# Performance work log

Hardware: AMD Instinct MI355X
Metric: run time of the kernel (lower is better)

Reference implementation:

```python
import jax, jax.numpy as jnp
import numpy as np

GRID_SIZE = 5
SPLINE_ORDER = 3
NUM_EXPERTS = 8
TOP_K = 2
CAP_FACTOR = 1.25
TEMP = 1.0
GDHW = (4, 4, 4)


def make_grid(in_features):
    # efficient-KAN grid buffer: grid_range=[-1,1], extended by spline_order on each side
    h = 2.0 / GRID_SIZE
    g = jnp.arange(-SPLINE_ORDER, GRID_SIZE + SPLINE_ORDER + 1, dtype=jnp.float32) * h - 1.0
    return jnp.broadcast_to(g, (in_features, g.shape[0]))


def b_splines(x, grid):
    # x: (N, in) -> (N, in, GRID_SIZE + SPLINE_ORDER) Cox-de Boor bases
    x = x[:, :, None]
    bases = ((x >= grid[:, :-1]) & (x < grid[:, 1:])).astype(x.dtype)
    for k in range(1, SPLINE_ORDER + 1):
        left = (x - grid[:, : -(k + 1)]) / (grid[:, k:-1] - grid[:, : -(k + 1)])
        right = (grid[:, k + 1:] - x) / (grid[:, k + 1:] - grid[:, 1:-k])
        bases = left * bases[:, :, :-1] + right * bases[:, :, 1:]
    return bases


def kan_linear(x, base_w, spline_w, scaler, grid):
    base = jax.nn.silu(x) @ base_w.T
    bs = b_splines(x, grid)                                   # (N, in, coef)
    spline = jnp.einsum('nic,oic->no', bs, spline_w * scaler[:, :, None])
    return base + spline


def layernorm(x, w, b, eps=1e-5):
    mu = x.mean(-1, keepdims=True)
    var = x.var(-1, keepdims=True)
    return (x - mu) / jnp.sqrt(var + eps) * w + b


def setup_inputs() -> dict:
    key = jax.random.key(0)
    ks = jax.random.split(key, 12)
    Cf, hidden, E, nc = 256, 170, NUM_EXPERTS, 2
    coef = GRID_SIZE + SPLINE_ORDER
    def nrm(k, shape, scale):
        return jax.random.normal(k, shape, dtype=jnp.float32) * scale
    return {
        'fpn_feat': nrm(ks[0], (8, 254, 32, 32, 32), 1.0),
        'seg_logits': nrm(ks[1], (8, 2, 32, 32, 32), 1.0),
        'ln_r_w': jnp.ones((Cf,), jnp.float32),
        'ln_r_b': jnp.zeros((Cf,), jnp.float32),
        'ln_h_w': jnp.ones((Cf,), jnp.float32),
        'ln_h_b': jnp.zeros((Cf,), jnp.float32),
        'router_w': nrm(ks[2], (E, Cf), Cf ** -0.5),
        'router_b': jnp.zeros((E,), jnp.float32),
        'bw1': nrm(ks[3], (E, hidden, Cf), Cf ** -0.5),
        'sw1': nrm(ks[4], (E, hidden, Cf, coef), 0.1 * Cf ** -0.5),
        'sc1': nrm(ks[5], (E, hidden, Cf), Cf ** -0.5),
        'bw2': nrm(ks[6], (E, Cf, hidden), hidden ** -0.5),
        'sw2': nrm(ks[7], (E, Cf, hidden, coef), 0.1 * hidden ** -0.5),
        'sc2': nrm(ks[8], (E, Cf, hidden), hidden ** -0.5),
        'cls_bw': nrm(ks[9], (nc, Cf), Cf ** -0.5),
        'cls_sw': nrm(ks[10], (nc, Cf, coef), 0.1 * Cf ** -0.5),
        'cls_sc': nrm(ks[11], (nc, Cf), Cf ** -0.5),
        'grid_cf': make_grid(Cf),
        'grid_hid': make_grid(hidden),
    }


def reference(fpn_feat, seg_logits, ln_r_w, ln_r_b, ln_h_w, ln_h_b,
              router_w, router_b, bw1, sw1, sc1, bw2, sw2, sc2,
              cls_bw, cls_sw, cls_sc, grid_cf, grid_hid):
    fused = jnp.concatenate([fpn_feat, seg_logits], axis=1)   # (B, Cf, D, H, W)
    B, C, D, H, W = fused.shape
    gd, gh, gw = GDHW
    dp, hp, wp = D // gd, H // gh, W // gw
    # split into gd*gh*gw blocks per sample
    blk = fused.reshape(B, C, gd, dp, gh, hp, gw, wp)
    blk = blk.transpose(0, 2, 4, 6, 1, 3, 5, 7).reshape(-1, C, dp, hp, wp)
    vec = blk.mean(axis=(2, 3, 4))                            # (N, Cf) global avg pool

    N = vec.shape[0]
    E = NUM_EXPERTS
    x_norm = layernorm(vec, ln_r_w, ln_r_b)
    scores = (x_norm @ router_w.T + router_b) / TEMP          # (N, E)
    top_val, top_idx = jax.lax.top_k(scores, TOP_K)
    top_w = jax.nn.softmax(top_val, axis=-1)
    capacity = int(CAP_FACTOR * N * TOP_K / E) + 1

    onehot = top_idx[None] == jnp.arange(E)[:, None, None]    # (E, N, K)
    sel = onehot.any(-1)                                      # (E, N)
    pos = jnp.cumsum(sel.astype(jnp.int32), axis=1)           # rank among selected (1-based)
    keep = sel & (pos <= capacity)                            # capacity drop = first-come order
    w = (top_w[None] * onehot.astype(top_w.dtype)).sum(-1)    # (E, N) combine weights

    def expert(bw1e, sw1e, sc1e, bw2e, sw2e, sc2e):
        h = kan_linear(x_norm, bw1e, sw1e, sc1e, grid_cf)
        h = jax.nn.gelu(h, approximate=False)                 # torch nn.GELU default (erf)
        return kan_linear(h, bw2e, sw2e, sc2e, grid_hid)

    y_all = jax.vmap(expert)(bw1, sw1, sc1, bw2, sw2, sc2)    # (E, N, Cf)
    out = jnp.einsum('en,enc->nc', keep.astype(vec.dtype) * w, y_all)

    conf = scores.max(-1)                                     # (N,)
    logits_blk = kan_linear(layernorm(out, ln_h_w, ln_h_b), cls_bw, cls_sw, cls_sc, grid_cf)
    P = gd * gh * gw
    weight = jax.nn.softmax(conf.reshape(B, P), axis=-1)[:, :, None]
    logits = (logits_blk.reshape(B, P, -1) * weight).sum(1)   # (B, num_classes)
    return logits
```

## Files before the change

### kernel.cpp

```cpp
#include <hip/hip_runtime.h>
#include <math.h>

#define CF 256
#define HID 170
#define NE 8
#define NTOK 512
#define K1 2304
#define K2P 1536
#define CAPACITY 161

typedef __bf16 bf16x8 __attribute__((ext_vector_type(8)));
typedef unsigned short u16x8 __attribute__((ext_vector_type(8)));
typedef float f32x4 __attribute__((ext_vector_type(4)));

__device__ __forceinline__ float silu_f(float x) { return x / (1.0f + expf(-x)); }
__device__ __forceinline__ float gelu_f(float x) {
    return 0.5f * x * (1.0f + erff(x * 0.70710678118654752f));
}

__device__ __forceinline__ unsigned short f2bf(float f) {
    unsigned int u = __float_as_uint(f);
    u = u + 0x7fffu + ((u >> 16) & 1u);
    return (unsigned short)(u >> 16);
}

__device__ __forceinline__ void gl_lds16(const unsigned short* g, unsigned short* l) {
    __builtin_amdgcn_global_load_lds(
        (const __attribute__((address_space(1))) unsigned int*)g,
        (__attribute__((address_space(3))) unsigned int*)l, 16, 0, 0);
}

__device__ __forceinline__ void bspline8(float x, float bs[8]) {
    float b[11];
#pragma unroll
    for (int j = 0; j < 11; ++j) {
        float g0 = (float)(j - 3) * 0.4f - 1.0f;
        float g1 = (float)(j - 2) * 0.4f - 1.0f;
        b[j] = (x >= g0 && x < g1) ? 1.0f : 0.0f;
    }
#pragma unroll
    for (int k = 1; k <= 3; ++k) {
        float inv = 2.5f / (float)k;
#pragma unroll
        for (int j = 0; j < 10 - (k - 1); ++j) {
            float gj   = (float)(j - 3) * 0.4f - 1.0f;
            float gjk1 = (float)(j - 2 + k) * 0.4f - 1.0f;
            b[j] = (x - gj) * inv * b[j] + (gjk1 - x) * inv * b[j + 1];
        }
    }
#pragma unroll
    for (int c = 0; c < 8; ++c) bs[c] = b[c];
}

__global__ __launch_bounds__(256) void mega_front_kernel(const float* __restrict__ fpn,
                                                         const float* __restrict__ seg,
                                                         const float* __restrict__ bw1,
                                                         const float* __restrict__ sw1,
                                                         const float* __restrict__ sc1,
                                                         const float* __restrict__ bw2,
                                                         const float* __restrict__ sw2,
                                                         const float* __restrict__ sc2,
                                                         float* __restrict__ vec,
                                                         unsigned short* __restrict__ W1,
                                                         unsigned short* __restrict__ W2,
                                                         float* __restrict__ out) {
    int id = blockIdx.x, tid = threadIdx.x;
    if (id == 2048 && tid < 16) out[tid] = 0.0f;
    if (id < 2048) {
        int c = id & 255, b = id >> 8;
        const float* src = (c < 254) ? fpn + (size_t)(b * 254 + c) * 32768
                                     : seg + (size_t)(b * 2 + (c - 254)) * 32768;
        const float4* s4 = (const float4*)src;
        float s[4] = {0.f, 0.f, 0.f, 0.f};
#pragma unroll
        for (int it = 0; it < 32; ++it) {
            float4 v = s4[it * 256 + tid];
            s[it >> 3] += v.x + v.y + v.z + v.w;
        }
        __shared__ float acc[64];
        if (tid < 64) acc[tid] = 0.0f;
        __syncthreads();
        int bh = tid >> 6, bw = (tid & 7) >> 1;
#pragma unroll
        for (int bd = 0; bd < 4; ++bd) atomicAdd(&acc[bd * 16 + bh * 4 + bw], s[bd]);
        __syncthreads();
        if (tid < 64) vec[(size_t)(b * 64 + tid) * CF + c] = acc[tid] * (1.0f / 512.0f);
    } else if (id < 2048 + NE * HID) {
        int r = id - 2048;
        int o = r % HID, e = r / HID, i = tid;
        size_t oi = (size_t)(e * HID + o) * CF + i;
        unsigned short* row = W1 + (size_t)(e * HID + o) * K1;
        row[i] = f2bf(bw1[oi]);
        float sc = sc1[oi];
        const float* sw = sw1 + oi * 8;
        u16x8 pk;
#pragma unroll
        for (int c = 0; c < 8; ++c) pk[c] = f2bf(sw[c] * sc);
        *(u16x8*)(row + CF + i * 8) = pk;
    } else {
        int r = id - (2048 + NE * HID);
        int o = r & 255, e = r >> 8, t = tid;
        unsigned short* row = W2 + (size_t)(e * CF + o) * K2P;
        if (t < HID) {
            size_t oi = (size_t)(e * CF + o) * HID + t;
            row[t] = f2bf(bw2[oi]);
            float sc = sc2[oi];
            const float* sw = sw2 + oi * 8;
            u16x8 pk;
#pragma unroll
            for (int c = 0; c < 8; ++c) pk[c] = f2bf(sw[c] * sc);
            *(u16x8*)(row + HID + t * 8) = pk;
        } else if (t < HID + 6) {
            row[HID * 9 + (t - HID)] = 0;
        }
    }
}

__global__ __launch_bounds__(256) void ln_score_a1_kernel(const float* __restrict__ vec,
                                                          const float* __restrict__ lnw,
                                                          const float* __restrict__ lnb,
                                                          const float* __restrict__ rw,
                                                          const float* __restrict__ rb,
                                                          float* __restrict__ scores,
                                                          unsigned short* __restrict__ A1,
                                                          unsigned short* __restrict__ A2) {
    int n = blockIdx.x, i = threadIdx.x;
    if (i < 48) {
        int e = i / 6, j = i - e * 6;
        A2[((size_t)e * NTOK + n) * K2P + HID * 9 + j] = 0;
    }
    float v = vec[(size_t)n * CF + i];
    float s1 = v, s2 = v * v;
#pragma unroll
    for (int off = 32; off > 0; off >>= 1) {
        s1 += __shfl_xor(s1, off);
        s2 += __shfl_xor(s2, off);
    }
    __shared__ float rs1[4], rs2[4];
    int lane = i & 63, wid = i >> 6;
    if (lane == 0) { rs1[wid] = s1; rs2[wid] = s2; }
    __syncthreads();
    float tot1 = rs1[0] + rs1[1] + rs1[2] + rs1[3];
    float tot2 = rs2[0] + rs2[1] + rs2[2] + rs2[3];
    float mu = tot1 * (1.0f / CF);
    float var = tot2 * (1.0f / CF) - mu * mu;
    float rsd = rsqrtf(var + 1e-5f);
    float xv = (v - mu) * rsd * lnw[i] + lnb[i];
    unsigned short* r = A1 + (size_t)n * K1;
    r[i] = f2bf(silu_f(xv));
    float bs[8]; bspline8(xv, bs);
    u16x8 pk;
#pragma unroll
    for (int c = 0; c < 8; ++c) pk[c] = f2bf(bs[c]);
    *(u16x8*)(r + CF + i * 8) = pk;
    float p[NE];
#pragma unroll
    for (int e = 0; e < NE; ++e) p[e] = xv * rw[e * CF + i];
#pragma unroll
    for (int off = 32; off > 0; off >>= 1)
#pragma unroll
        for (int e = 0; e < NE; ++e) p[e] += __shfl_xor(p[e], off);
    __shared__ float pacc[4][NE];
    if (lane == 0)
#pragma unroll
        for (int e = 0; e < NE; ++e) pacc[wid][e] = p[e];
    __syncthreads();
    if (i < NE)
        scores[n * NE + i] = pacc[0][i] + pacc[1][i] + pacc[2][i] + pacc[3][i] + rb[i];
}

__global__ __launch_bounds__(256) void gemm_mfma_kernel(
        const unsigned short* __restrict__ Ag, const unsigned short* __restrict__ Bg,
        float* __restrict__ C, unsigned short* __restrict__ A2,
        const float* __restrict__ scores, float* __restrict__ cw, float* __restrict__ conf,
        int N, int K, long sA, long sB, long sC, int ldc, int mode) {
    __shared__ alignas(16) unsigned short As[2][4096];
    __shared__ alignas(16) unsigned short Bs[2][4096];
    __shared__ int   ti0[NTOK], ti1[NTOK];
    __shared__ float tw0[NTOK], tw1[NTOK];

    int tid = threadIdx.x;
    if (mode == 1 && blockIdx.x == 3) {
        if (blockIdx.y != 0 || blockIdx.z != 0) return;
        int lane = tid & 63, w4 = tid >> 6;
#pragma unroll
        for (int half = 0; half < 2; ++half) {
            int n = half * 256 + tid;
            float m1 = -1e30f, m2 = -1e30f; int i1 = 0, i2 = 0;
#pragma unroll
            for (int e = 0; e < NE; ++e) {
                float sc = scores[n * NE + e];
                if (sc > m1) { m2 = m1; i2 = i1; m1 = sc; i1 = e; }
                else if (sc > m2) { m2 = sc; i2 = e; }
            }
            conf[n] = m1;
            float ew = expf(m2 - m1);
            ti0[n] = i1; ti1[n] = i2;
            tw0[n] = 1.0f / (1.0f + ew); tw1[n] = ew / (1.0f + ew);
        }
        __syncthreads();
#pragma unroll
        for (int e2 = 0; e2 < 2; ++e2) {
            int e = w4 * 2 + e2;
            int cnt = 0;
#pragma unroll
            for (int c = 0; c < NTOK / 64; ++c) {
                int t = c * 64 + lane;
                int h0 = (ti0[t] == e), h1 = (ti1[t] == e);
                int sel = h0 | h1;
                unsigned long long mask = __ballot(sel);
                int pos = cnt + (int)__popcll(mask & ((1ull << lane) - 1ull));
                float wv = 0.f;
                if (sel && pos < CAPACITY) wv = h0 ? tw0[t] : tw1[t];
                cw[e * NTOK + t] = wv;
                cnt += (int)__popcll(mask);
            }
        }
        return;
    }

    int e = blockIdx.z;
    const unsigned short* A = Ag + (size_t)e * sA;
    const unsigned short* B = Bg + (size_t)e * sB;
    int m0 = blockIdx.y * 64, n0 = blockIdx.x * 64;
    int lane = tid & 63, w = tid >> 6;
    int wr = w >> 1, wc = w & 1;
    int fr = lane & 15, fg = lane >> 4;
    int lrow = lane >> 3, lch = lane & 7;
    int csw = (lch ^ lrow) * 8;

    const unsigned short* aS0 = A + (size_t)(m0 + w * 16 + lrow) * K + csw;
    const unsigned short* aS1 = aS0 + (size_t)8 * K;
    const unsigned short* bS0 = B + (size_t)(n0 + w * 16 + lrow) * K + csw;
    const unsigned short* bS1 = bS0 + (size_t)8 * K;
    unsigned short* dA0[2] = {&As[0][(w * 16) * 64], &As[1][(w * 16) * 64]};
    unsigned short* dA1[2] = {&As[0][(w * 16 + 8) * 64], &As[1][(w * 16 + 8) * 64]};
    unsigned short* dB0[2] = {&Bs[0][(w * 16) * 64], &Bs[1][(w * 16) * 64]};
    unsigned short* dB1[2] = {&Bs[0][(w * 16 + 8) * 64], &Bs[1][(w * 16 + 8) * 64]};

#define STAGE(bi, k0)                 \
    gl_lds16(aS0 + (k0), dA0[bi]);    \
    gl_lds16(aS1 + (k0), dA1[bi]);    \
    gl_lds16(bS0 + (k0), dB0[bi]);    \
    gl_lds16(bS1 + (k0), dB1[bi]);

    f32x4 acc[2][2];
#pragma unroll
    for (int i = 0; i < 2; ++i)
#pragma unroll
        for (int j = 0; j < 2; ++j)
#pragma unroll
            for (int r = 0; r < 4; ++r) acc[i][j][r] = 0.f;

    const int steps = K >> 6;
    STAGE(0, 0);
    for (int s = 0; s < steps; ++s) {
        int bi = s & 1;
        if (s + 1 < steps) {
            STAGE(bi ^ 1, (s + 1) << 6);
            asm volatile("s_waitcnt vmcnt(4)" ::: "memory");
        } else {
            asm volatile("s_waitcnt vmcnt(0)" ::: "memory");
        }
        __builtin_amdgcn_s_barrier();
        asm volatile("" ::: "memory");
        const unsigned char* Ab = (const unsigned char*)As[bi];
        const unsigned char* Bb = (const unsigned char*)Bs[bi];
#pragma unroll
        for (int ks = 0; ks < 2; ++ks) {
            int kb = ks * 64 + fg * 16;
            u16x8 af[2], bf[2];
#pragma unroll
            for (int mf = 0; mf < 2; ++mf) {
                int row = wr * 32 + mf * 16 + fr;
                af[mf] = *(const u16x8*)(Ab + row * 128 + (kb ^ ((row & 7) << 4)));
            }
#pragma unroll
            for (int nf = 0; nf < 2; ++nf) {
                int row = wc * 32 + nf * 16 + fr;
                bf[nf] = *(const u16x8*)(Bb + row * 128 + (kb ^ ((row & 7) << 4)));
            }
#pragma unroll
            for (int mf = 0; mf < 2; ++mf)
#pragma unroll
                for (int nf = 0; nf < 2; ++nf)
                    acc[mf][nf] = __builtin_amdgcn_mfma_f32_16x16x32_bf16(
                        __builtin_bit_cast(bf16x8, af[mf]),
                        __builtin_bit_cast(bf16x8, bf[nf]), acc[mf][nf], 0, 0, 0);
        }
        asm volatile("" ::: "memory");
        __builtin_amdgcn_s_barrier();
        asm volatile("" ::: "memory");
    }
#undef STAGE

    if (mode == 1) {
#pragma unroll
        for (int mf = 0; mf < 2; ++mf)
#pragma unroll
            for (int nf = 0; nf < 2; ++nf)
#pragma unroll
                for (int r = 0; r < 4; ++r) {
                    int row = m0 + wr * 32 + mf * 16 + fg * 4 + r;
                    int col = n0 + wc * 32 + nf * 16 + fr;
                    if (col < N) {
                        float g = gelu_f(acc[mf][nf][r]);
                        unsigned short* rr = A2 + ((size_t)e * NTOK + row) * K2P;
                        rr[col] = f2bf(silu_f(g));
                        float bs[8]; bspline8(g, bs);
                        u16x8 pk;
#pragma unroll
                        for (int c = 0; c < 8; ++c) pk[c] = f2bf(bs[c]);
                        *(u16x8*)(rr + HID + col * 8) = pk;
                    }
                }
    } else {
        float* Ce = C + (size_t)e * sC;
#pragma unroll
        for (int mf = 0; mf < 2; ++mf)
#pragma unroll
            for (int nf = 0; nf < 2; ++nf)
#pragma unroll
                for (int r = 0; r < 4; ++r) {
                    int row = m0 + wr * 32 + mf * 16 + fg * 4 + r;
                    int col = n0 + wc * 32 + nf * 16 + fr;
                    if (col < N) Ce[(size_t)row * ldc + col] = acc[mf][nf][r];
                }
    }
}

__global__ __launch_bounds__(256) void combcls_kernel(const float* __restrict__ y,
                                                      const float* __restrict__ cw,
                                                      const float* __restrict__ conf,
                                                      const float* __restrict__ lnw,
                                                      const float* __restrict__ lnb,
                                                      const float* __restrict__ cbw,
                                                      const float* __restrict__ csw,
                                                      const float* __restrict__ csc,
                                                      float* __restrict__ out) {
    int n = blockIdx.x, i = threadIdx.x;
    float v = 0.f;
#pragma unroll
    for (int e = 0; e < NE; ++e)
        v += cw[e * NTOK + n] * y[((size_t)(e * NTOK + n)) * CF + i];
    float s1 = v, s2 = v * v;
#pragma unroll
    for (int off = 32; off > 0; off >>= 1) {
        s1 += __shfl_xor(s1, off);
        s2 += __shfl_xor(s2, off);
    }
    __shared__ float rA[4], rB[4], rP0[4], rP1[4];
    int lane = i & 63, wid = i >> 6;
    if (lane == 0) { rA[wid] = s1; rB[wid] = s2; }
    __syncthreads();
    float tot1 = rA[0] + rA[1] + rA[2] + rA[3];
    float tot2 = rB[0] + rB[1] + rB[2] + rB[3];
    float mu = tot1 * (1.0f / CF);
    float var = tot2 * (1.0f / CF) - mu * mu;
    float rs = rsqrtf(var + 1e-5f);
    float xh = (v - mu) * rs * lnw[i] + lnb[i];
    float si = silu_f(xh);
    float bs[8]; bspline8(xh, bs);
    float p0 = si * cbw[i], p1 = si * cbw[CF + i];
    float sp0 = 0.f, sp1 = 0.f;
#pragma unroll
    for (int c = 0; c < 8; ++c) {
        sp0 += bs[c] * csw[(size_t)i * 8 + c];
        sp1 += bs[c] * csw[(size_t)(CF + i) * 8 + c];
    }
    p0 += sp0 * csc[i];
    p1 += sp1 * csc[CF + i];
#pragma unroll
    for (int off = 32; off > 0; off >>= 1) {
        p0 += __shfl_xor(p0, off);
        p1 += __shfl_xor(p1, off);
    }
    if (lane == 0) { rP0[wid] = p0; rP1[wid] = p1; }
// ... 15 lines not shown
            atomicAdd(&out[b * 2 + 0], wself * l0);
            atomicAdd(&out[b * 2 + 1], wself * l1);
        }
    }
}

extern "C" void kernel_launch(void* const* d_in, const int* in_sizes, int n_in,
                              void* d_out, int out_size, void* d_ws, size_t ws_size,
                              hipStream_t stream) {
    const float* fpn      = (const float*)d_in[0];
    const float* seg      = (const float*)d_in[1];
    const float* ln_r_w   = (const float*)d_in[2];
    const float* ln_r_b   = (const float*)d_in[3];
    const float* ln_h_w   = (const float*)d_in[4];
    const float* ln_h_b   = (const float*)d_in[5];
    const float* router_w = (const float*)d_in[6];
    const float* router_b = (const float*)d_in[7];
    const float* bw1      = (const float*)d_in[8];
    const float* sw1      = (const float*)d_in[9];
    const float* sc1      = (const float*)d_in[10];
    const float* bw2      = (const float*)d_in[11];
    const float* sw2      = (const float*)d_in[12];
    const float* sc2      = (const float*)d_in[13];
    const float* cls_bw   = (const float*)d_in[14];
    const float* cls_sw   = (const float*)d_in[15];
    const float* cls_sc   = (const float*)d_in[16];
    float* out = (float*)d_out;

    float* ws = (float*)d_ws;
    float* vec    = ws;
    float* scores = vec + 131072;
    float* cw     = scores + 4096;
    float* conf   = cw + 4096;
    float* yall   = conf + 512;
    unsigned short* A1b = (unsigned short*)(yall + 1048576);
    unsigned short* W1b = A1b + (size_t)NTOK * K1;
    unsigned short* A2b = W1b + (size_t)NE * HID * K1;
    unsigned short* W2b = A2b + (size_t)NE * NTOK * K2P;

    mega_front_kernel<<<dim3(2048 + NE * HID + 2048), dim3(256), 0, stream>>>(
        fpn, seg, bw1, sw1, sc1, bw2, sw2, sc2, vec, W1b, W2b, out);
    ln_score_a1_kernel<<<dim3(NTOK), dim3(256), 0, stream>>>(vec, ln_r_w, ln_r_b, router_w,
                                                             router_b, scores, A1b, A2b);
    gemm_mfma_kernel<<<dim3(4, 8, NE), dim3(256), 0, stream>>>(
        A1b, W1b, nullptr, A2b, scores, cw, conf, HID, K1, 0L, (long)HID * K1, 0L, 0, 1);
    gemm_mfma_kernel<<<dim3(4, 8, NE), dim3(256), 0, stream>>>(
        A2b, W2b, yall, nullptr, nullptr, nullptr, nullptr, CF, K2P, (long)NTOK * K2P,
        (long)CF * K2P, (long)NTOK * CF, CF, 0);
    combcls_kernel<<<dim3(NTOK), dim3(256), 0, stream>>>(yall, cw, conf, ln_h_w, ln_h_b,
                                                         cls_bw, cls_sw, cls_sc, out);
}
```

Before: 133.3 us.

## Split-K expert GEMMs in halves and move routing into last LN block

Both expert GEMMs now split K into two halves across the z grid dimension, which doubles the block count. Each half writes fp32 partials. In the first GEMM, the second-arriving block (found with an atomic counter) sums both halves and applies GELU plus B-spline expansion. The second GEMM's halves are summed inside the combine kernel. The top-2 routing and capacity computation moves out of a GEMM block into the last-finishing block of the LN/score kernel. The GEMM staging switches from direct global-to-LDS loads to register prefetch with single-buffered LDS. The aim is better CU occupancy on the small GEMMs, at the cost of extra partial-sum traffic, atomics and threadfences.

```diff
diff --git a/kernel.cpp b/kernel.cpp
--- a/kernel.cpp
+++ b/kernel.cpp
@@ -8,6 +8,8 @@
 #define K1 2304
 #define K2P 1536
 #define CAPACITY 161
+#define KH1 1152
+#define KH2 768
 
 typedef __bf16 bf16x8 __attribute__((ext_vector_type(8)));
 typedef unsigned short u16x8 __attribute__((ext_vector_type(8)));
@@ -22,12 +24,6 @@
     unsigned int u = __float_as_uint(f);
     u = u + 0x7fffu + ((u >> 16) & 1u);
     return (unsigned short)(u >> 16);
-}
-
-__device__ __forceinline__ void gl_lds16(const unsigned short* g, unsigned short* l) {
-    __builtin_amdgcn_global_load_lds(
-        (const __attribute__((address_space(1))) unsigned int*)g,
-        (__attribute__((address_space(3))) unsigned int*)l, 16, 0, 0);
 }
 
 __device__ __forceinline__ void bspline8(float x, float bs[8]) {
@@ -63,9 +59,13 @@
                                                          float* __restrict__ vec,
                                                          unsigned short* __restrict__ W1,
                                                          unsigned short* __restrict__ W2,
+                                                         int* __restrict__ cnts,
                                                          float* __restrict__ out) {
     int id = blockIdx.x, tid = threadIdx.x;
-    if (id == 2048 && tid < 16) out[tid] = 0.0f;
+    if (id == 2048) {
+        if (tid < 16) out[tid] = 0.0f;
+        cnts[tid] = 0;
+    }
     if (id < 2048) {
         int c = id & 255, b = id >> 8;
         const float* src = (c < 254) ? fpn + (size_t)(b * 254 + c) * 32768
@@ -123,7 +123,10 @@
                                                           const float* __restrict__ rb,
                                                           float* __restrict__ scores,
                                                           unsigned short* __restrict__ A1,
-                                                          unsigned short* __restrict__ A2) {
+                                                          unsigned short* __restrict__ A2,
+                                                          int* __restrict__ lncnt,
+                                                          float* __restrict__ cw,
+                                                          float* __restrict__ conf) {
     int n = blockIdx.x, i = threadIdx.x;
     if (i < 48) {
         int e = i / 6, j = i - e * 6;
@@ -167,82 +170,75 @@
     __syncthreads();
     if (i < NE)
         scores[n * NE + i] = pacc[0][i] + pacc[1][i] + pacc[2][i] + pacc[3][i] + rb[i];
+    __syncthreads();
+    __shared__ int lastf;
+    if (i == 0) {
+        __threadfence();
+        lastf = (atomicAdd(lncnt, 1) == NTOK - 1);
+        __threadfence();
+    }
+    __syncthreads();
+    if (!lastf) return;
+    __shared__ int   ti0[NTOK], ti1[NTOK];
+    __shared__ float tw0[NTOK], tw1[NTOK];
+#pragma unroll
+    for (int half = 0; half < 2; ++half) {
+        int t = half * 256 + i;
+        float m1 = -1e30f, m2 = -1e30f; int i1 = 0, i2 = 0;
+#pragma unroll
+        for (int e = 0; e < NE; ++e) {
+            float sc = scores[t * NE + e];
+            if (sc > m1) { m2 = m1; i2 = i1; m1 = sc; i1 = e; }
+            else if (sc > m2) { m2 = sc; i2 = e; }
+        }
+        conf[t] = m1;
+        float ew = expf(m2 - m1);
+        ti0[t] = i1; ti1[t] = i2;
+        tw0[t] = 1.0f / (1.0f + ew); tw1[t] = ew / (1.0f + ew);
+    }
+    __syncthreads();
+    int w4 = i >> 6;
+#pragma unroll
+    for (int e2 = 0; e2 < 2; ++e2) {
+        int e = w4 * 2 + e2;
+        int cnt = 0;
+#pragma unroll
+        for (int c = 0; c < NTOK / 64; ++c) {
+            int t = c * 64 + lane;
+            int h0 = (ti0[t] == e), h1 = (ti1[t] == e);
+            int sel = h0 | h1;
+            unsigned long long mask = __ballot(sel);
+            int pos = cnt + (int)__popcll(mask & ((1ull << lane) - 1ull));
+            float wv = 0.f;
+            if (sel && pos < CAPACITY) wv = h0 ? tw0[t] : tw1[t];
+            cw[e * NTOK + t] = wv;
+            cnt += (int)__popcll(mask);
+        }
+    }
 }
 
 __global__ __launch_bounds__(256) void gemm_mfma_kernel(
         const unsigned short* __restrict__ Ag, const unsigned short* __restrict__ Bg,
-        float* __restrict__ C, unsigned short* __restrict__ A2,
-        const float* __restrict__ scores, float* __restrict__ cw, float* __restrict__ conf,
-        int N, int K, long sA, long sB, long sC, int ldc, int mode) {
-    __shared__ alignas(16) unsigned short As[2][4096];
-    __shared__ alignas(16) unsigned short Bs[2][4096];
-    __shared__ int   ti0[NTOK], ti1[NTOK];
-    __shared__ float tw0[NTOK], tw1[NTOK];
+        float* __restrict__ Ppart, unsigned short* __restrict__ A2,
+        int* __restrict__ cnt, int N, int LD, long sA, long sB, long pStride,
+        int khalf, int mode) {
+    int z = blockIdx.z, e = z >> 1, half = z & 1;
+    int koff = half * khalf, steps = khalf >> 6;
+    const unsigned short* A = Ag + (size_t)e * sA + koff;
+    const unsigned short* B = Bg + (size_t)e * sB + koff;
+    int m0 = blockIdx.y * 64, n0 = blockIdx.x * 64;
+
+    __shared__ alignas(16) unsigned char AsB[8192];
+    __shared__ alignas(16) unsigned char BsB[8192];
 
     int tid = threadIdx.x;
-    if (mode == 1 && blockIdx.x == 3) {
-        if (blockIdx.y != 0 || blockIdx.z != 0) return;
-        int lane = tid & 63, w4 = tid >> 6;
-#pragma unroll
-        for (int half = 0; half < 2; ++half) {
-            int n = half * 256 + tid;
-            float m1 = -1e30f, m2 = -1e30f; int i1 = 0, i2 = 0;
-#pragma unroll
-            for (int e = 0; e < NE; ++e) {
-                float sc = scores[n * NE + e];
-                if (sc > m1) { m2 = m1; i2 = i1; m1 = sc; i1 = e; }
-                else if (sc > m2) { m2 = sc; i2 = e; }
-            }
-            conf[n] = m1;
-            float ew = expf(m2 - m1);
-            ti0[n] = i1; ti1[n] = i2;
-            tw0[n] = 1.0f / (1.0f + ew); tw1[n] = ew / (1.0f + ew);
-        }
-        __syncthreads();
-#pragma unroll
-        for (int e2 = 0; e2 < 2; ++e2) {
-            int e = w4 * 2 + e2;
-            int cnt = 0;
-#pragma unroll
-            for (int c = 0; c < NTOK / 64; ++c) {
-                int t = c * 64 + lane;
-                int h0 = (ti0[t] == e), h1 = (ti1[t] == e);
-                int sel = h0 | h1;
-                unsigned long long mask = __ballot(sel);
-                int pos = cnt + (int)__popcll(mask & ((1ull << lane) - 1ull));
-                float wv = 0.f;
-                if (sel && pos < CAPACITY) wv = h0 ? tw0[t] : tw1[t];
-                cw[e * NTOK + t] = wv;
-                cnt += (int)__popcll(mask);
-            }
-        }
-        return;
-    }
-
-    int e = blockIdx.z;
-    const unsigned short* A = Ag + (size_t)e * sA;
-    const unsigned short* B = Bg + (size_t)e * sB;
-    int m0 = blockIdx.y * 64, n0 = blockIdx.x * 64;
     int lane = tid & 63, w = tid >> 6;
     int wr = w >> 1, wc = w & 1;
     int fr = lane & 15, fg = lane >> 4;
-    int lrow = lane >> 3, lch = lane & 7;
-    int csw = (lch ^ lrow) * 8;
-
-    const unsigned short* aS0 = A + (size_t)(m0 + w * 16 + lrow) * K + csw;
-    const unsigned short* aS1 = aS0 + (size_t)8 * K;
-    const unsigned short* bS0 = B + (size_t)(n0 + w * 16 + lrow) * K + csw;
-    const unsigned short* bS1 = bS0 + (size_t)8 * K;
-    unsigned short* dA0[2] = {&As[0][(w * 16) * 64], &As[1][(w * 16) * 64]};
-    unsigned short* dA1[2] = {&As[0][(w * 16 + 8) * 64], &As[1][(w * 16 + 8) * 64]};
-    unsigned short* dB0[2] = {&Bs[0][(w * 16) * 64], &Bs[1][(w * 16) * 64]};
-    unsigned short* dB1[2] = {&Bs[0][(w * 16 + 8) * 64], &Bs[1][(w * 16 + 8) * 64]};
-
-#define STAGE(bi, k0)                 \
-    gl_lds16(aS0 + (k0), dA0[bi]);    \
-    gl_lds16(aS1 + (k0), dA1[bi]);    \
-    gl_lds16(bS0 + (k0), dB0[bi]);    \
-    gl_lds16(bS1 + (k0), dB1[bi]);
+    int srow = tid >> 3, schunk = tid & 7;
+    int r0 = srow, r1 = srow + 32;
+    int wb0 = r0 * 128 + ((schunk * 16) ^ ((r0 & 7) << 4));
+    int wb1 = r1 * 128 + ((schunk * 16) ^ ((r1 & 7) << 4));
 
     f32x4 acc[2][2];
 #pragma unroll
@@ -252,20 +248,32 @@
 #pragma unroll
             for (int r = 0; r < 4; ++r) acc[i][j][r] = 0.f;
 
-    const int steps = K >> 6;
-    STAGE(0, 0);
+    int bn0 = n0 + r0, bn1 = n0 + r1;
+    const unsigned short* Ar0 = A + (size_t)(m0 + r0) * LD + schunk * 8;
+    const unsigned short* Ar1 = A + (size_t)(m0 + r1) * LD + schunk * 8;
+    const unsigned short* Br0 = B + (size_t)bn0 * LD + schunk * 8;
+    const unsigned short* Br1 = B + (size_t)bn1 * LD + schunk * 8;
+    u16x8 a0, a1, b0, b1;
+    a0 = *(const u16x8*)Ar0;
+    a1 = *(const u16x8*)Ar1;
+    b0 = b1 = (u16x8){0, 0, 0, 0, 0, 0, 0, 0};
+    if (bn0 < N) b0 = *(const u16x8*)Br0;
+    if (bn1 < N) b1 = *(const u16x8*)Br1;
+
     for (int s = 0; s < steps; ++s) {
-        int bi = s & 1;
+        __syncthreads();
+        *(u16x8*)(AsB + wb0) = a0;
+        *(u16x8*)(AsB + wb1) = a1;
+        *(u16x8*)(BsB + wb0) = b0;
+        *(u16x8*)(BsB + wb1) = b1;
+        __syncthreads();
         if (s + 1 < steps) {
-            STAGE(bi ^ 1, (s + 1) << 6);
-            asm volatile("s_waitcnt vmcnt(4)" ::: "memory");
-        } else {
-            asm volatile("s_waitcnt vmcnt(0)" ::: "memory");
-        }
-        __builtin_amdgcn_s_barrier();
-        asm volatile("" ::: "memory");
-        const unsigned char* Ab = (const unsigned char*)As[bi];
-        const unsigned char* Bb = (const unsigned char*)Bs[bi];
+            int k0 = (s + 1) << 6;
+            a0 = *(const u16x8*)(Ar0 + k0);
+            a1 = *(const u16x8*)(Ar1 + k0);
+            if (bn0 < N) b0 = *(const u16x8*)(Br0 + k0);
+            if (bn1 < N) b1 = *(const u16x8*)(Br1 + k0);
+        }
 #pragma unroll
         for (int ks = 0; ks < 2; ++ks) {
             int kb = ks * 64 + fg * 16;
@@ -273,12 +281,12 @@
 #pragma unroll
             for (int mf = 0; mf < 2; ++mf) {
                 int row = wr * 32 + mf * 16 + fr;
-                af[mf] = *(const u16x8*)(Ab + row * 128 + (kb ^ ((row & 7) << 4)));
+                af[mf] = *(const u16x8*)(AsB + row * 128 + (kb ^ ((row & 7) << 4)));
             }
 #pragma unroll
             for (int nf = 0; nf < 2; ++nf) {
                 int row = wc * 32 + nf * 16 + fr;
-                bf[nf] = *(const u16x8*)(Bb + row * 128 + (kb ^ ((row & 7) << 4)));
+                bf[nf] = *(const u16x8*)(BsB + row * 128 + (kb ^ ((row & 7) << 4)));
             }
 #pragma unroll
             for (int mf = 0; mf < 2; ++mf)
@@ -288,48 +296,55 @@
                         __builtin_bit_cast(bf16x8, af[mf]),
                         __builtin_bit_cast(bf16x8, bf[nf]), acc[mf][nf], 0, 0, 0);
         }
-        asm volatile("" ::: "memory");
-        __builtin_amdgcn_s_barrier();
-        asm volatile("" ::: "memory");
-    }
-#undef STAGE
-
-    if (mode == 1) {
-#pragma unroll
-        for (int mf = 0; mf < 2; ++mf)
-#pragma unroll
-            for (int nf = 0; nf < 2; ++nf)
-#pragma unroll
-                for (int r = 0; r < 4; ++r) {
-                    int row = m0 + wr * 32 + mf * 16 + fg * 4 + r;
-                    int col = n0 + wc * 32 + nf * 16 + fr;
-                    if (col < N) {
-                        float g = gelu_f(acc[mf][nf][r]);
-                        unsigned short* rr = A2 + ((size_t)e * NTOK + row) * K2P;
-                        rr[col] = f2bf(silu_f(g));
-                        float bs[8]; bspline8(g, bs);
-                        u16x8 pk;
-#pragma unroll
-                        for (int c = 0; c < 8; ++c) pk[c] = f2bf(bs[c]);
-                        *(u16x8*)(rr + HID + col * 8) = pk;
-                    }
+    }
+
+    float* P = Ppart + (size_t)half * pStride + (size_t)e * NTOK * N;
+#pragma unroll
+    for (int mf = 0; mf < 2; ++mf)
+#pragma unroll
+        for (int nf = 0; nf < 2; ++nf)
+#pragma unroll
+            for (int r = 0; r < 4; ++r) {
+                int row = m0 + wr * 32 + mf * 16 + fg * 4 + r;
+                int col = n0 + wc * 32 + nf * 16 + fr;
+                if (col < N) P[(size_t)row * N + col] = acc[mf][nf][r];
+            }
+    if (mode == 0) return;
+
+    __syncthreads();
+    __shared__ int lastf;
+    int tix = e * 24 + blockIdx.y * 3 + blockIdx.x;
+    if (tid == 0) {
+        __threadfence();
+        lastf = (atomicAdd(&cnt[tix], 1) == 1);
+        __threadfence();
+    }
+    __syncthreads();
+    if (!lastf) return;
+    const float* Q = Ppart + (size_t)(half ^ 1) * pStride + (size_t)e * NTOK * N;
+#pragma unroll
+    for (int mf = 0; mf < 2; ++mf)
+#pragma unroll
+        for (int nf = 0; nf < 2; ++nf)
+#pragma unroll
+            for (int r = 0; r < 4; ++r) {
+                int row = m0 + wr * 32 + mf * 16 + fg * 4 + r;
+                int col = n0 + wc * 32 + nf * 16 + fr;
+                if (col < N) {
+                    float g = gelu_f(acc[mf][nf][r] + Q[(size_t)row * N + col]);
+                    unsigned short* rr = A2 + ((size_t)e * NTOK + row) * K2P;
+                    rr[col] = f2bf(silu_f(g));
+                    float bs[8]; bspline8(g, bs);
+                    u16x8 pk;
+#pragma unroll
+                    for (int c = 0; c < 8; ++c) pk[c] = f2bf(bs[c]);
+                    *(u16x8*)(rr + HID + col * 8) = pk;
                 }
-    } else {
-        float* Ce = C + (size_t)e * sC;
-#pragma unroll
-        for (int mf = 0; mf < 2; ++mf)
-#pragma unroll
-            for (int nf = 0; nf < 2; ++nf)
-#pragma unroll
-                for (int r = 0; r < 4; ++r) {
-                    int row = m0 + wr * 32 + mf * 16 + fg * 4 + r;
-                    int col = n0 + wc * 32 + nf * 16 + fr;
-                    if (col < N) Ce[(size_t)row * ldc + col] = acc[mf][nf][r];
-                }
-    }
-}
-
-__global__ __launch_bounds__(256) void combcls_kernel(const float* __restrict__ y,
+            }
+}
+
+__global__ __launch_bounds__(256) void combcls_kernel(const float* __restrict__ y0,
+                                                      const float* __restrict__ y1,
                                                       const float* __restrict__ cw,
                                                       const float* __restrict__ conf,
                                                       const float* __restrict__ lnw,
@@ -341,8 +356,10 @@
     int n = blockIdx.x, i = threadIdx.x;
     float v = 0.f;
 #pragma unroll
-    for (int e = 0; e < NE; ++e)
-        v += cw[e * NTOK + n] * y[((size_t)(e * NTOK + n)) * CF + i];
+    for (int e = 0; e < NE; ++e) {
+        size_t idx = ((size_t)(e * NTOK + n)) * CF + i;
+        v += cw[e * NTOK + n] * (y0[idx] + y1[idx]);
+    }
     float s1 = v, s2 = v * v;
 #pragma unroll
     for (int off = 32; off > 0; off >>= 1) {
@@ -424,21 +441,25 @@
     float* scores = vec + 131072;
     float* cw     = scores + 4096;
     float* conf   = cw + 4096;
-    float* yall   = conf + 512;
-    unsigned short* A1b = (unsigned short*)(yall + 1048576);
+    int*   cnts   = (int*)(conf + 512);
+    float* Hpart  = (float*)(cnts + 256);
+    float* Ypart  = Hpart + 2 * (size_t)NE * NTOK * HID;
+    unsigned short* A1b = (unsigned short*)(Ypart + 2 * (size_t)NE * NTOK * CF);
     unsigned short* W1b = A1b + (size_t)NTOK * K1;
     unsigned short* A2b = W1b + (size_t)NE * HID * K1;
     unsigned short* W2b = A2b + (size_t)NE * NTOK * K2P;
 
     mega_front_kernel<<<dim3(2048 + NE * HID + 2048), dim3(256), 0, stream>>>(
-        fpn, seg, bw1, sw1, sc1, bw2, sw2, sc2, vec, W1b, W2b, out);
-    ln_score_a1_kernel<<<dim3(NTOK), dim3(256), 0, stream>>>(vec, ln_r_w, ln_r_b, router_w,
-                                                             router_b, scores, A1b, A2b);
-    gemm_mfma_kernel<<<dim3(4, 8, NE), dim3(256), 0, stream>>>(
-        A1b, W1b, nullptr, A2b, scores, cw, conf, HID, K1, 0L, (long)HID * K1, 0L, 0, 1);
-    gemm_mfma_kernel<<<dim3(4, 8, NE), dim3(256), 0, stream>>>(
-        A2b, W2b, yall, nullptr, nullptr, nullptr, nullptr, CF, K2P, (long)NTOK * K2P,
-        (long)CF * K2P, (long)NTOK * CF, CF, 0);
-    combcls_kernel<<<dim3(NTOK), dim3(256), 0, stream>>>(yall, cw, conf, ln_h_w, ln_h_b,
-                                                         cls_bw, cls_sw, cls_sc, out);
-}
+        fpn, seg, bw1, sw1, sc1, bw2, sw2, sc2, vec, W1b, W2b, cnts, out);
+    ln_score_a1_kernel<<<dim3(NTOK), dim3(256), 0, stream>>>(
+        vec, ln_r_w, ln_r_b, router_w, router_b, scores, A1b, A2b, cnts + 192, cw, conf);
+    gemm_mfma_kernel<<<dim3(3, 8, 16), dim3(256), 0, stream>>>(
+        A1b, W1b, Hpart, A2b, cnts, HID, K1, 0L, (long)HID * K1,
+        (long)NE * NTOK * HID, KH1, 1);
+    gemm_mfma_kernel<<<dim3(4, 8, 16), dim3(256), 0, stream>>>(
+        A2b, W2b, Ypart, nullptr, nullptr, CF, K2P, (long)NTOK * K2P, (long)CF * K2P,
+        (long)NE * NTOK * CF, KH2, 0);
+    combcls_kernel<<<dim3(NTOK), dim3(256), 0, stream>>>(
+        Ypart, Ypart + (size_t)NE * NTOK * CF, cw, conf, ln_h_w, ln_h_b, cls_bw, cls_sw,
+        cls_sc, out);
+}
```

Measured after the change: 168.3 us. +26.2%, slower.

## Retile expert GEMMs to 32x64 blocks with register-staged loads

Applied to the files above, without the earlier changes.

Reshapes both expert GEMMs from 64x64 tiles with 256 threads to 32x64 tiles with 128 threads on a flat 1D grid. This gives more blocks to fill the GPU's compute units and removes the wasted fourth column tile in the first GEMM, where N is 170. The direct global-to-LDS async loads with a double buffer are replaced by register prefetch into a single LDS buffer, with two barriers per k-step. The kernel is templated on mode, and routing now runs in one extra block. The trade-offs are more barriers, no LDS double buffering, and more total A-tile reloads.

```diff
diff --git a/kernel.cpp b/kernel.cpp
--- a/kernel.cpp
+++ b/kernel.cpp
@@ -22,12 +22,6 @@
     unsigned int u = __float_as_uint(f);
     u = u + 0x7fffu + ((u >> 16) & 1u);
     return (unsigned short)(u >> 16);
-}
-
-__device__ __forceinline__ void gl_lds16(const unsigned short* g, unsigned short* l) {
-    __builtin_amdgcn_global_load_lds(
-        (const __attribute__((address_space(1))) unsigned int*)g,
-        (__attribute__((address_space(3))) unsigned int*)l, 16, 0, 0);
 }
 
 __device__ __forceinline__ void bspline8(float x, float bs[8]) {
@@ -169,39 +163,40 @@
         scores[n * NE + i] = pacc[0][i] + pacc[1][i] + pacc[2][i] + pacc[3][i] + rb[i];
 }
 
-__global__ __launch_bounds__(256) void gemm_mfma_kernel(
+template <int MODE>
+__global__ __launch_bounds__(128) void gemm_mfma_kernel(
         const unsigned short* __restrict__ Ag, const unsigned short* __restrict__ Bg,
         float* __restrict__ C, unsigned short* __restrict__ A2,
         const float* __restrict__ scores, float* __restrict__ cw, float* __restrict__ conf,
-        int N, int K, long sA, long sB, long sC, int ldc, int mode) {
-    __shared__ alignas(16) unsigned short As[2][4096];
-    __shared__ alignas(16) unsigned short Bs[2][4096];
-    __shared__ int   ti0[NTOK], ti1[NTOK];
-    __shared__ float tw0[NTOK], tw1[NTOK];
-
-    int tid = threadIdx.x;
-    if (mode == 1 && blockIdx.x == 3) {
-        if (blockIdx.y != 0 || blockIdx.z != 0) return;
-        int lane = tid & 63, w4 = tid >> 6;
-#pragma unroll
-        for (int half = 0; half < 2; ++half) {
-            int n = half * 256 + tid;
+        int N, int K, long sA, long sB, long sC, int ldc, int ntx, int grid_main) {
+    __shared__ alignas(16) unsigned char smem[12288];
+    int bid = blockIdx.x, tid = threadIdx.x;
+    int lane = tid & 63, w = tid >> 6;
+
+    if (MODE == 1 && bid >= grid_main) {
+        int* ti0 = (int*)smem;
+        int* ti1 = ti0 + NTOK;
+        float* tw0 = (float*)(ti1 + NTOK);
+        float* tw1 = tw0 + NTOK;
+#pragma unroll
+        for (int q = 0; q < 4; ++q) {
+            int t = q * 128 + tid;
             float m1 = -1e30f, m2 = -1e30f; int i1 = 0, i2 = 0;
 #pragma unroll
             for (int e = 0; e < NE; ++e) {
-                float sc = scores[n * NE + e];
+                float sc = scores[t * NE + e];
                 if (sc > m1) { m2 = m1; i2 = i1; m1 = sc; i1 = e; }
                 else if (sc > m2) { m2 = sc; i2 = e; }
             }
-            conf[n] = m1;
+            conf[t] = m1;
             float ew = expf(m2 - m1);
-            ti0[n] = i1; ti1[n] = i2;
-            tw0[n] = 1.0f / (1.0f + ew); tw1[n] = ew / (1.0f + ew);
+            ti0[t] = i1; ti1[t] = i2;
+            tw0[t] = 1.0f / (1.0f + ew); tw1[t] = ew / (1.0f + ew);
         }
         __syncthreads();
 #pragma unroll
-        for (int e2 = 0; e2 < 2; ++e2) {
-            int e = w4 * 2 + e2;
+        for (int eh = 0; eh < 4; ++eh) {
+            int e = w * 4 + eh;
             int cnt = 0;
 #pragma unroll
             for (int c = 0; c < NTOK / 64; ++c) {
@@ -219,30 +214,33 @@
         return;
     }
 
-    int e = blockIdx.z;
-    const unsigned short* A = Ag + (size_t)e * sA;
-    const unsigned short* B = Bg + (size_t)e * sB;
-    int m0 = blockIdx.y * 64, n0 = blockIdx.x * 64;
-    int lane = tid & 63, w = tid >> 6;
-    int wr = w >> 1, wc = w & 1;
+    int tpe = 16 * ntx;
+    int e = bid / tpe, rem = bid % tpe;
+    int m0 = (rem / ntx) * 32, n0 = (rem % ntx) * 64;
+    const unsigned short* A = Ag + (size_t)e * sA + (size_t)m0 * K;
+    const unsigned short* B = Bg + (size_t)e * sB + (size_t)n0 * K;
+
+    unsigned char* AsB = smem;
+    unsigned char* BsB = smem + 4096;
+
     int fr = lane & 15, fg = lane >> 4;
-    int lrow = lane >> 3, lch = lane & 7;
-    int csw = (lch ^ lrow) * 8;
-
-    const unsigned short* aS0 = A + (size_t)(m0 + w * 16 + lrow) * K + csw;
-    const unsigned short* aS1 = aS0 + (size_t)8 * K;
-    const unsigned short* bS0 = B + (size_t)(n0 + w * 16 + lrow) * K + csw;
-    const unsigned short* bS1 = bS0 + (size_t)8 * K;
-    unsigned short* dA0[2] = {&As[0][(w * 16) * 64], &As[1][(w * 16) * 64]};
-    unsigned short* dA1[2] = {&As[0][(w * 16 + 8) * 64], &As[1][(w * 16 + 8) * 64]};
-    unsigned short* dB0[2] = {&Bs[0][(w * 16) * 64], &Bs[1][(w * 16) * 64]};
-    unsigned short* dB1[2] = {&Bs[0][(w * 16 + 8) * 64], &Bs[1][(w * 16 + 8) * 64]};
-
-#define STAGE(bi, k0)                 \
-    gl_lds16(aS0 + (k0), dA0[bi]);    \
-    gl_lds16(aS1 + (k0), dA1[bi]);    \
-    gl_lds16(bS0 + (k0), dB0[bi]);    \
-    gl_lds16(bS1 + (k0), dB1[bi]);
+    int aw[2], bw[4];
+    const unsigned short* aSrc[2];
+    const unsigned short* bSrc[4];
+    bool bOk[4];
+#pragma unroll
+    for (int q = 0; q < 2; ++q) {
+        int c = tid + q * 128, r = c >> 3, ch = c & 7;
+        aw[q] = r * 128 + ((ch * 16) ^ ((r & 7) << 4));
+        aSrc[q] = A + (size_t)r * K + ch * 8;
+    }
+#pragma unroll
+    for (int q = 0; q < 4; ++q) {
+        int c = tid + q * 128, r = c >> 3, ch = c & 7;
+        bw[q] = r * 128 + ((ch * 16) ^ ((r & 7) << 4));
+        bSrc[q] = B + (size_t)r * K + ch * 8;
+        bOk[q] = (n0 + r) < N;
+    }
 
     f32x4 acc[2][2];
 #pragma unroll
@@ -253,32 +251,41 @@
             for (int r = 0; r < 4; ++r) acc[i][j][r] = 0.f;
 
     const int steps = K >> 6;
-    STAGE(0, 0);
+    u16x8 pa[2], pb[4];
+#pragma unroll
+    for (int q = 0; q < 2; ++q) pa[q] = *(const u16x8*)aSrc[q];
+#pragma unroll
+    for (int q = 0; q < 4; ++q)
+        pb[q] = bOk[q] ? *(const u16x8*)bSrc[q] : (u16x8){0, 0, 0, 0, 0, 0, 0, 0};
+
     for (int s = 0; s < steps; ++s) {
-        int bi = s & 1;
+        __syncthreads();
+#pragma unroll
+        for (int q = 0; q < 2; ++q) *(u16x8*)(AsB + aw[q]) = pa[q];
+#pragma unroll
+        for (int q = 0; q < 4; ++q) *(u16x8*)(BsB + bw[q]) = pb[q];
+        __syncthreads();
         if (s + 1 < steps) {
-            STAGE(bi ^ 1, (s + 1) << 6);
-            asm volatile("s_waitcnt vmcnt(4)" ::: "memory");
-        } else {
-            asm volatile("s_waitcnt vmcnt(0)" ::: "memory");
-        }
-        __builtin_amdgcn_s_barrier();
-        asm volatile("" ::: "memory");
-        const unsigned char* Ab = (const unsigned char*)As[bi];
-        const unsigned char* Bb = (const unsigned char*)Bs[bi];
+            int k0 = (s + 1) << 6;
+#pragma unroll
+            for (int q = 0; q < 2; ++q) pa[q] = *(const u16x8*)(aSrc[q] + k0);
+#pragma unroll
+            for (int q = 0; q < 4; ++q)
+                if (bOk[q]) pb[q] = *(const u16x8*)(bSrc[q] + k0);
+        }
 #pragma unroll
         for (int ks = 0; ks < 2; ++ks) {
             int kb = ks * 64 + fg * 16;
             u16x8 af[2], bf[2];
 #pragma unroll
             for (int mf = 0; mf < 2; ++mf) {
-                int row = wr * 32 + mf * 16 + fr;
-                af[mf] = *(const u16x8*)(Ab + row * 128 + (kb ^ ((row & 7) << 4)));
+                int row = mf * 16 + fr;
+                af[mf] = *(const u16x8*)(AsB + row * 128 + (kb ^ ((row & 7) << 4)));
             }
 #pragma unroll
             for (int nf = 0; nf < 2; ++nf) {
-                int row = wc * 32 + nf * 16 + fr;
-                bf[nf] = *(const u16x8*)(Bb + row * 128 + (kb ^ ((row & 7) << 4)));
+                int row = w * 32 + nf * 16 + fr;
+                bf[nf] = *(const u16x8*)(BsB + row * 128 + (kb ^ ((row & 7) << 4)));
             }
 #pragma unroll
             for (int mf = 0; mf < 2; ++mf)
@@ -288,21 +295,17 @@
                         __builtin_bit_cast(bf16x8, af[mf]),
                         __builtin_bit_cast(bf16x8, bf[nf]), acc[mf][nf], 0, 0, 0);
         }
-        asm volatile("" ::: "memory");
-        __builtin_amdgcn_s_barrier();
-        asm volatile("" ::: "memory");
-    }
-#undef STAGE
-
-    if (mode == 1) {
+    }
+
+    if (MODE == 1) {
 #pragma unroll
         for (int mf = 0; mf < 2; ++mf)
 #pragma unroll
             for (int nf = 0; nf < 2; ++nf)
 #pragma unroll
                 for (int r = 0; r < 4; ++r) {
-                    int row = m0 + wr * 32 + mf * 16 + fg * 4 + r;
-                    int col = n0 + wc * 32 + nf * 16 + fr;
+                    int row = m0 + mf * 16 + fg * 4 + r;
+                    int col = n0 + w * 32 + nf * 16 + fr;
                     if (col < N) {
                         float g = gelu_f(acc[mf][nf][r]);
                         unsigned short* rr = A2 + ((size_t)e * NTOK + row) * K2P;
@@ -322,8 +325,8 @@
             for (int nf = 0; nf < 2; ++nf)
 #pragma unroll
                 for (int r = 0; r < 4; ++r) {
-                    int row = m0 + wr * 32 + mf * 16 + fg * 4 + r;
-                    int col = n0 + wc * 32 + nf * 16 + fr;
+                    int row = m0 + mf * 16 + fg * 4 + r;
+                    int col = n0 + w * 32 + nf * 16 + fr;
                     if (col < N) Ce[(size_t)row * ldc + col] = acc[mf][nf][r];
                 }
     }
@@ -434,11 +437,12 @@
         fpn, seg, bw1, sw1, sc1, bw2, sw2, sc2, vec, W1b, W2b, out);
     ln_score_a1_kernel<<<dim3(NTOK), dim3(256), 0, stream>>>(vec, ln_r_w, ln_r_b, router_w,
                                                              router_b, scores, A1b, A2b);
-    gemm_mfma_kernel<<<dim3(4, 8, NE), dim3(256), 0, stream>>>(
-        A1b, W1b, nullptr, A2b, scores, cw, conf, HID, K1, 0L, (long)HID * K1, 0L, 0, 1);
-    gemm_mfma_kernel<<<dim3(4, 8, NE), dim3(256), 0, stream>>>(
+    gemm_mfma_kernel<1><<<dim3(385), dim3(128), 0, stream>>>(
+        A1b, W1b, nullptr, A2b, scores, cw, conf, HID, K1, 0L, (long)HID * K1, 0L, 0,
+        3, 384);
+    gemm_mfma_kernel<0><<<dim3(512), dim3(128), 0, stream>>>(
         A2b, W2b, yall, nullptr, nullptr, nullptr, nullptr, CF, K2P, (long)NTOK * K2P,
-        (long)CF * K2P, (long)NTOK * CF, CF, 0);
+        (long)CF * K2P, (long)NTOK * CF, CF, 4, 512);
     combcls_kernel<<<dim3(NTOK), dim3(256), 0, stream>>>(yall, cw, conf, ln_h_w, ln_h_b,
                                                          cls_bw, cls_sw, cls_sc, out);
 }
```

Result: no change. 131.0 us (-1.7%).

## Replace direct global-to-LDS loads with register-staged double-buffered GEMM pipeline

Applied to the files above, without the earlier changes.

The GEMM kernel stops using global_load_lds direct-to-LDS copies. It now loads tiles into registers two steps ahead and writes them to swizzled LDS buffers, unrolling the main loop by two so the next tile's loads overlap the current tile's MFMA work. The kernel becomes a template on MODE so the routing branch is resolved at compile time, and shared memory is merged into one aliased buffer. The B rows past N are now zero-filled behind a bounds check instead of being read past the end. This costs more VGPRs, adds LDS write instructions, and assumes the step count is even.

```diff
diff --git a/kernel.cpp b/kernel.cpp
--- a/kernel.cpp
+++ b/kernel.cpp
@@ -22,12 +22,6 @@
     unsigned int u = __float_as_uint(f);
     u = u + 0x7fffu + ((u >> 16) & 1u);
     return (unsigned short)(u >> 16);
-}
-
-__device__ __forceinline__ void gl_lds16(const unsigned short* g, unsigned short* l) {
-    __builtin_amdgcn_global_load_lds(
-        (const __attribute__((address_space(1))) unsigned int*)g,
-        (__attribute__((address_space(3))) unsigned int*)l, 16, 0, 0);
 }
 
 __device__ __forceinline__ void bspline8(float x, float bs[8]) {
@@ -169,39 +163,41 @@
         scores[n * NE + i] = pacc[0][i] + pacc[1][i] + pacc[2][i] + pacc[3][i] + rb[i];
 }
 
+template <int MODE>
 __global__ __launch_bounds__(256) void gemm_mfma_kernel(
         const unsigned short* __restrict__ Ag, const unsigned short* __restrict__ Bg,
         float* __restrict__ C, unsigned short* __restrict__ A2,
         const float* __restrict__ scores, float* __restrict__ cw, float* __restrict__ conf,
-        int N, int K, long sA, long sB, long sC, int ldc, int mode) {
-    __shared__ alignas(16) unsigned short As[2][4096];
-    __shared__ alignas(16) unsigned short Bs[2][4096];
-    __shared__ int   ti0[NTOK], ti1[NTOK];
-    __shared__ float tw0[NTOK], tw1[NTOK];
-
+        int N, int K, long sA, long sB, long sC, int ldc) {
+    __shared__ alignas(16) unsigned char smem[32768];
     int tid = threadIdx.x;
-    if (mode == 1 && blockIdx.x == 3) {
+    int lane = tid & 63, w = tid >> 6;
+
+    if (MODE == 1 && blockIdx.x == 3) {
         if (blockIdx.y != 0 || blockIdx.z != 0) return;
-        int lane = tid & 63, w4 = tid >> 6;
+        int* ti0 = (int*)smem;
+        int* ti1 = ti0 + NTOK;
+        float* tw0 = (float*)(ti1 + NTOK);
+        float* tw1 = tw0 + NTOK;
 #pragma unroll
         for (int half = 0; half < 2; ++half) {
-            int n = half * 256 + tid;
+            int t = half * 256 + tid;
             float m1 = -1e30f, m2 = -1e30f; int i1 = 0, i2 = 0;
 #pragma unroll
             for (int e = 0; e < NE; ++e) {
-                float sc = scores[n * NE + e];
+                float sc = scores[t * NE + e];
                 if (sc > m1) { m2 = m1; i2 = i1; m1 = sc; i1 = e; }
                 else if (sc > m2) { m2 = sc; i2 = e; }
             }
-            conf[n] = m1;
+            conf[t] = m1;
             float ew = expf(m2 - m1);
-            ti0[n] = i1; ti1[n] = i2;
-            tw0[n] = 1.0f / (1.0f + ew); tw1[n] = ew / (1.0f + ew);
+            ti0[t] = i1; ti1[t] = i2;
+            tw0[t] = 1.0f / (1.0f + ew); tw1[t] = ew / (1.0f + ew);
         }
         __syncthreads();
 #pragma unroll
         for (int e2 = 0; e2 < 2; ++e2) {
-            int e = w4 * 2 + e2;
+            int e = w * 2 + e2;
             int cnt = 0;
 #pragma unroll
             for (int c = 0; c < NTOK / 64; ++c) {
@@ -219,30 +215,27 @@
         return;
     }
 
+    unsigned char* As0 = smem;
+    unsigned char* As1 = smem + 8192;
+    unsigned char* Bs0 = smem + 16384;
+    unsigned char* Bs1 = smem + 24576;
+
     int e = blockIdx.z;
     const unsigned short* A = Ag + (size_t)e * sA;
     const unsigned short* B = Bg + (size_t)e * sB;
     int m0 = blockIdx.y * 64, n0 = blockIdx.x * 64;
-    int lane = tid & 63, w = tid >> 6;
     int wr = w >> 1, wc = w & 1;
     int fr = lane & 15, fg = lane >> 4;
-    int lrow = lane >> 3, lch = lane & 7;
-    int csw = (lch ^ lrow) * 8;
-
-    const unsigned short* aS0 = A + (size_t)(m0 + w * 16 + lrow) * K + csw;
-    const unsigned short* aS1 = aS0 + (size_t)8 * K;
-    const unsigned short* bS0 = B + (size_t)(n0 + w * 16 + lrow) * K + csw;
-    const unsigned short* bS1 = bS0 + (size_t)8 * K;
-    unsigned short* dA0[2] = {&As[0][(w * 16) * 64], &As[1][(w * 16) * 64]};
-    unsigned short* dA1[2] = {&As[0][(w * 16 + 8) * 64], &As[1][(w * 16 + 8) * 64]};
-    unsigned short* dB0[2] = {&Bs[0][(w * 16) * 64], &Bs[1][(w * 16) * 64]};
-    unsigned short* dB1[2] = {&Bs[0][(w * 16 + 8) * 64], &Bs[1][(w * 16 + 8) * 64]};
-
-#define STAGE(bi, k0)                 \
-    gl_lds16(aS0 + (k0), dA0[bi]);    \
-    gl_lds16(aS1 + (k0), dA1[bi]);    \
-    gl_lds16(bS0 + (k0), dB0[bi]);    \
-    gl_lds16(bS1 + (k0), dB1[bi]);
+    int srow = tid >> 3, schunk = tid & 7;
+    int r0 = srow, r1 = srow + 32;
+    int wb0 = r0 * 128 + ((schunk * 16) ^ ((r0 & 7) << 4));
+    int wb1 = r1 * 128 + ((schunk * 16) ^ ((r1 & 7) << 4));
+    int bn0 = n0 + r0, bn1 = n0 + r1;
+    const unsigned short* Ar0 = A + (size_t)(m0 + r0) * K + schunk * 8;
+    const unsigned short* Ar1 = A + (size_t)(m0 + r1) * K + schunk * 8;
+    const unsigned short* Br0 = B + (size_t)bn0 * K + schunk * 8;
+    const unsigned short* Br1 = B + (size_t)bn1 * K + schunk * 8;
+    const u16x8 zero8 = {0, 0, 0, 0, 0, 0, 0, 0};
 
     f32x4 acc[2][2];
 #pragma unroll
@@ -252,49 +245,77 @@
 #pragma unroll
             for (int r = 0; r < 4; ++r) acc[i][j][r] = 0.f;
 
+    u16x8 pa0, pa1, pb0, pb1;
+    u16x8 qa0, qa1, qb0, qb1;
+
+#define LOADP(k0)                                                   \
+    pa0 = *(const u16x8*)(Ar0 + (k0));                              \
+    pa1 = *(const u16x8*)(Ar1 + (k0));                              \
+    pb0 = (bn0 < N) ? *(const u16x8*)(Br0 + (k0)) : zero8;          \
+    pb1 = (bn1 < N) ? *(const u16x8*)(Br1 + (k0)) : zero8;
+#define LOADQ(k0)                                                   \
+    qa0 = *(const u16x8*)(Ar0 + (k0));                              \
+    qa1 = *(const u16x8*)(Ar1 + (k0));                              \
+    qb0 = (bn0 < N) ? *(const u16x8*)(Br0 + (k0)) : zero8;          \
+    qb1 = (bn1 < N) ? *(const u16x8*)(Br1 + (k0)) : zero8;
+#define STP(Abuf, Bbuf)                                             \
+    *(u16x8*)(Abuf + wb0) = pa0; *(u16x8*)(Abuf + wb1) = pa1;       \
+    *(u16x8*)(Bbuf + wb0) = pb0; *(u16x8*)(Bbuf + wb1) = pb1;
+#define STQ(Abuf, Bbuf)                                             \
+    *(u16x8*)(Abuf + wb0) = qa0; *(u16x8*)(Abuf + wb1) = qa1;       \
+    *(u16x8*)(Bbuf + wb0) = qb0; *(u16x8*)(Bbuf + wb1) = qb1;
+#define LBAR()                                                      \
+    asm volatile("s_waitcnt lgkmcnt(0)" ::: "memory");              \
+    __builtin_amdgcn_s_barrier();
+#define COMPUTE(Abuf, Bbuf)                                         \
+    _Pragma("unroll")                                               \
+    for (int ks = 0; ks < 2; ++ks) {                                \
+        int kb = ks * 64 + fg * 16;                                 \
+        u16x8 af[2], bf[2];                                         \
+        _Pragma("unroll")                                           \
+        for (int mf = 0; mf < 2; ++mf) {                            \
+            int row = wr * 32 + mf * 16 + fr;                       \
+            af[mf] = *(const u16x8*)(Abuf + row * 128 + (kb ^ ((row & 7) << 4))); \
+        }                                                           \
+        _Pragma("unroll")                                           \
+        for (int nf = 0; nf < 2; ++nf) {                            \
+            int row = wc * 32 + nf * 16 + fr;                       \
+            bf[nf] = *(const u16x8*)(Bbuf + row * 128 + (kb ^ ((row & 7) << 4))); \
+        }                                                           \
+        _Pragma("unroll")                                           \
+        for (int mf = 0; mf < 2; ++mf)                              \
+            _Pragma("unroll")                                       \
+            for (int nf = 0; nf < 2; ++nf)                          \
+                acc[mf][nf] = __builtin_amdgcn_mfma_f32_16x16x32_bf16( \
+                    __builtin_bit_cast(bf16x8, af[mf]),             \
+                    __builtin_bit_cast(bf16x8, bf[nf]), acc[mf][nf], 0, 0, 0); \
+    }
+
     const int steps = K >> 6;
-    STAGE(0, 0);
-    for (int s = 0; s < steps; ++s) {
-        int bi = s & 1;
-        if (s + 1 < steps) {
-            STAGE(bi ^ 1, (s + 1) << 6);
-            asm volatile("s_waitcnt vmcnt(4)" ::: "memory");
-        } else {
-            asm volatile("s_waitcnt vmcnt(0)" ::: "memory");
-        }
-        __builtin_amdgcn_s_barrier();
-        asm volatile("" ::: "memory");
-        const unsigned char* Ab = (const unsigned char*)As[bi];
-        const unsigned char* Bb = (const unsigned char*)Bs[bi];
-#pragma unroll
-        for (int ks = 0; ks < 2; ++ks) {
-            int kb = ks * 64 + fg * 16;
-            u16x8 af[2], bf[2];
-#pragma unroll
-            for (int mf = 0; mf < 2; ++mf) {
-                int row = wr * 32 + mf * 16 + fr;
-                af[mf] = *(const u16x8*)(Ab + row * 128 + (kb ^ ((row & 7) << 4)));
-            }
-#pragma unroll
-            for (int nf = 0; nf < 2; ++nf) {
-                int row = wc * 32 + nf * 16 + fr;
-                bf[nf] = *(const u16x8*)(Bb + row * 128 + (kb ^ ((row & 7) << 4)));
-            }
-#pragma unroll
-            for (int mf = 0; mf < 2; ++mf)
-#pragma unroll
-                for (int nf = 0; nf < 2; ++nf)
-                    acc[mf][nf] = __builtin_amdgcn_mfma_f32_16x16x32_bf16(
-                        __builtin_bit_cast(bf16x8, af[mf]),
-                        __builtin_bit_cast(bf16x8, bf[nf]), acc[mf][nf], 0, 0, 0);
-        }
-        asm volatile("" ::: "memory");
-        __builtin_amdgcn_s_barrier();
-        asm volatile("" ::: "memory");
-    }
-#undef STAGE
-
-    if (mode == 1) {
+    LOADP(0);
+    LOADQ(64);
+    STP(As0, Bs0);
+    LBAR();
+    for (int s = 0; s < steps; s += 2) {
+        STQ(As1, Bs1);
+        if (s + 2 < steps) { LOADP((s + 2) << 6); }
+        COMPUTE(As0, Bs0);
+        LBAR();
+        if (s + 2 < steps) {
+            STP(As0, Bs0);
+            if (s + 3 < steps) { LOADQ((s + 3) << 6); }
+        }
+        COMPUTE(As1, Bs1);
+        if (s + 2 < steps) { LBAR(); }
+    }
+#undef LOADP
+#undef LOADQ
+#undef STP
+#undef STQ
+#undef LBAR
+#undef COMPUTE
+
+    if (MODE == 1) {
 #pragma unroll
         for (int mf = 0; mf < 2; ++mf)
 #pragma unroll
@@ -434,11 +455,11 @@
         fpn, seg, bw1, sw1, sc1, bw2, sw2, sc2, vec, W1b, W2b, out);
     ln_score_a1_kernel<<<dim3(NTOK), dim3(256), 0, stream>>>(vec, ln_r_w, ln_r_b, router_w,
                                                              router_b, scores, A1b, A2b);
-    gemm_mfma_kernel<<<dim3(4, 8, NE), dim3(256), 0, stream>>>(
-        A1b, W1b, nullptr, A2b, scores, cw, conf, HID, K1, 0L, (long)HID * K1, 0L, 0, 1);
-    gemm_mfma_kernel<<<dim3(4, 8, NE), dim3(256), 0, stream>>>(
+    gemm_mfma_kernel<1><<<dim3(4, 8, NE), dim3(256), 0, stream>>>(
+        A1b, W1b, nullptr, A2b, scores, cw, conf, HID, K1, 0L, (long)HID * K1, 0L, 0);
+    gemm_mfma_kernel<0><<<dim3(4, 8, NE), dim3(256), 0, stream>>>(
         A2b, W2b, yall, nullptr, nullptr, nullptr, nullptr, CF, K2P, (long)NTOK * K2P,
-        (long)CF * K2P, (long)NTOK * CF, CF, 0);
+        (long)CF * K2P, (long)NTOK * CF, CF);
     combcls_kernel<<<dim3(NTOK), dim3(256), 0, stream>>>(yall, cw, conf, ln_h_w, ln_h_b,
                                                          cls_bw, cls_sw, cls_sc, out);
 }
```

Result: faster. 121.4 us (-8.9%).
